# Optimization experiments

Measured on AMD Instinct MI355X. Metric: run time of the kernel, lower is better.

## Reference

```python
import jax, jax.numpy as jnp
import numpy as np

N = 32768      # total nodes
B = 64         # graphs
NPG = 512      # nodes per graph
E = 524288     # edges (avg degree 16)
H = 4          # heads
Fh = 64        # per-head dim
C = H * Fh     # 256
FIN = 128
RATIO = 0.5


def gat(x, src, dst, W, a_src, a_dst, bias, n_nodes):
    # PyG GATConv: linear -> add self-loops -> edge softmax over dst -> scatter-add
    h = (x @ W).reshape(n_nodes, H, Fh)
    loop = jnp.arange(n_nodes)
    s = jnp.concatenate([src, loop])
    d = jnp.concatenate([dst, loop])
    es = jnp.sum(h * a_src, axis=-1)  # [N,H]
    ed = jnp.sum(h * a_dst, axis=-1)  # [N,H]
    e = jax.nn.leaky_relu(es[s] + ed[d], 0.2)  # [E+N,H]
    m = jax.ops.segment_max(e, d, num_segments=n_nodes)
    ex = jnp.exp(e - m[d])
    den = jax.ops.segment_sum(ex, d, num_segments=n_nodes)
    alpha = ex / (den[d] + 1e-16)  # [E+N,H]
    out = jax.ops.segment_sum(alpha[:, :, None] * h[s], d, num_segments=n_nodes)
    return out.reshape(n_nodes, C) + bias


def pool(x, sw, sb, tw, tb, n_graphs, n_per):
    # equal-size graphs -> per-graph top-k as a batched top_k
    k = max(1, int(n_per * RATIO))
    scores = jax.nn.sigmoid(x @ sw + sb)[:, 0].reshape(n_graphs, n_per)
    _, idx = jax.lax.top_k(scores, k)  # [B,k]
    xb = x.reshape(n_graphs, n_per, x.shape[-1])
    sel = jnp.take_along_axis(xb, idx[:, :, None], axis=1)
    sel = sel.reshape(n_graphs * k, x.shape[-1])
    return sel @ tw + tb, k


def setup_inputs() -> dict:
    key = jax.random.key(0)
    ks = jax.random.split(key, 24)
    x = jax.random.normal(ks[0], (N, FIN), dtype=jnp.float32)
    # within-graph random edges
    gbase = jnp.repeat(jnp.arange(B, dtype=jnp.int32) * NPG, E // B)
    src = gbase + jax.random.randint(ks[1], (E,), 0, NPG)
    dst = gbase + jax.random.randint(ks[2], (E,), 0, NPG)
    edge_index = jnp.stack([src, dst]).astype(jnp.int32)
    batch = jnp.repeat(jnp.arange(B, dtype=jnp.int32), NPG)
    def lin(k, fi, fo):
        return jax.random.normal(k, (fi, fo), dtype=jnp.float32) / np.sqrt(fi)
    inp = dict(x=x, edge_index=edge_index, batch=batch)
    inp["W1"] = lin(ks[3], FIN, C)
    inp["a_src1"] = jax.random.normal(ks[4], (H, Fh), jnp.float32) / np.sqrt(Fh)
    inp["a_dst1"] = jax.random.normal(ks[5], (H, Fh), jnp.float32) / np.sqrt(Fh)
    inp["b1"] = jnp.zeros((C,), jnp.float32)
    inp["W2"] = lin(ks[6], C, C)
    inp["a_src2"] = jax.random.normal(ks[7], (H, Fh), jnp.float32) / np.sqrt(Fh)
    inp["a_dst2"] = jax.random.normal(ks[8], (H, Fh), jnp.float32) / np.sqrt(Fh)
    inp["b2"] = jnp.zeros((C,), jnp.float32)
    inp["p1_sw"] = lin(ks[9], C, 1)
    inp["p1_sb"] = jnp.zeros((1,), jnp.float32)
    inp["p1_tw"] = lin(ks[10], C, C)
    inp["p1_tb"] = jnp.zeros((C,), jnp.float32)
    inp["p2_sw"] = lin(ks[11], C, 1)
    inp["p2_sb"] = jnp.zeros((1,), jnp.float32)
    inp["p2_tw"] = lin(ks[12], C, C)
    inp["p2_tb"] = jnp.zeros((C,), jnp.float32)
    inp["c1w"] = lin(ks[13], C, 64)
    inp["c1b"] = jnp.zeros((64,), jnp.float32)
    inp["c2w"] = lin(ks[14], 64, 2)
    inp["c2b"] = jnp.zeros((2,), jnp.float32)
    return inp


def reference(x, edge_index, batch, W1, a_src1, a_dst1, b1, W2, a_src2, a_dst2, b2,
              p1_sw, p1_sb, p1_tw, p1_tb, p2_sw, p2_sb, p2_tw, p2_tb,
              c1w, c1b, c2w, c2b):
    src, dst = edge_index[0], edge_index[1]
    h = jax.nn.elu(gat(x, src, dst, W1, a_src1, a_dst1, b1, N))
    h = jax.nn.elu(gat(h, src, dst, W2, a_src2, a_dst2, b2, N))
    # pool1 then pool2 (edge_index after pooling is never consumed by the output path)
    h, k1 = pool(h, p1_sw, p1_sb, p1_tw, p1_tb, B, NPG)
    h, k2 = pool(h, p2_sw, p2_sb, p2_tw, p2_tb, B, k1)
    g = h.reshape(B, k2, C).mean(axis=1)  # global mean pool per graph
    g = jax.nn.relu(g @ c1w + c1b)
    g = g @ c2w + c2b
    return jax.nn.log_softmax(g, axis=1)
```

## Files before the change

### kernel.cpp

```cpp
#include <hip/hip_runtime.h>
#include <hip/hip_bf16.h>
#include <hip/hip_fp16.h>
#include <math.h>

constexpr int NN  = 32768;
constexpr int BG  = 64;
constexpr int NPG = 512;
constexpr int EG  = 524288;
constexpr int EPG = EG / BG;
constexpr int HH  = 4;
constexpr int FH  = 64;
constexpr int CC  = 256;
constexpr int FIN = 128;
constexpr int KP1 = 256;
constexpr int KP2 = 128;
constexpr int NS  = 4;

typedef __attribute__((ext_vector_type(8))) short short8;
typedef __attribute__((ext_vector_type(4))) float f32x4;

__device__ inline float leaky02(float v) { return v > 0.0f ? v : 0.2f * v; }

__device__ inline unsigned short f2bf(float v) {
    __hip_bfloat16 h = __float2bfloat16(v);
    return *(unsigned short*)&h;
}
__device__ inline float bf2f(unsigned short u) {
    __hip_bfloat16 h;
    *(unsigned short*)&h = u;
    return __bfloat162float(h);
}
__device__ inline void split2(float v, unsigned short& hi, unsigned short& lo) {
    hi = f2bf(v);
    lo = f2bf(v - bf2f(hi));
}
__device__ inline void split8(const float* p, short8& hi, short8& lo) {
    const float4 f0 = *(const float4*)p;
    const float4 f1 = *(const float4*)(p + 4);
    unsigned short h, l;
    split2(f0.x, h, l); hi[0] = (short)h; lo[0] = (short)l;
    split2(f0.y, h, l); hi[1] = (short)h; lo[1] = (short)l;
    split2(f0.z, h, l); hi[2] = (short)h; lo[2] = (short)l;
    split2(f0.w, h, l); hi[3] = (short)h; lo[3] = (short)l;
    split2(f1.x, h, l); hi[4] = (short)h; lo[4] = (short)l;
    split2(f1.y, h, l); hi[5] = (short)h; lo[5] = (short)l;
    split2(f1.z, h, l); hi[6] = (short)h; lo[6] = (short)l;
    split2(f1.w, h, l); hi[7] = (short)h; lo[7] = (short)l;
}

__device__ inline unsigned short f2h(float v) {
    __half h = __float2half(v);
    return *(unsigned short*)&h;
}

__device__ inline void acc8h(const unsigned short* p, float a, float* acc) {
    const uint4 u = *(const uint4*)p;
    const __half2* hp = (const __half2*)&u;
    const float2 f0 = __half22float2(hp[0]);
    const float2 f1 = __half22float2(hp[1]);
    const float2 f2 = __half22float2(hp[2]);
    const float2 f3 = __half22float2(hp[3]);
    acc[0] = fmaf(a, f0.x, acc[0]); acc[1] = fmaf(a, f0.y, acc[1]);
    acc[2] = fmaf(a, f1.x, acc[2]); acc[3] = fmaf(a, f1.y, acc[3]);
    acc[4] = fmaf(a, f2.x, acc[4]); acc[5] = fmaf(a, f2.y, acc[5]);
    acc[6] = fmaf(a, f3.x, acc[6]); acc[7] = fmaf(a, f3.y, acc[7]);
}

__global__ __launch_bounds__(1024) void setup_k(
        const int* __restrict__ src, const int* __restrict__ dst,
        int* __restrict__ rowp, int* __restrict__ esrc,
        const float* __restrict__ tw1, const float* __restrict__ sw2,
        const float* __restrict__ tb1, const float* __restrict__ sb2,
        float* __restrict__ w12, float* __restrict__ b12,
        const float* __restrict__ tw2, const float* __restrict__ c1w,
        const float* __restrict__ tb2, float* __restrict__ T,
        float* __restrict__ bc2,
        const float* __restrict__ W1, const float* __restrict__ W2,
        unsigned short* __restrict__ w1ph, unsigned short* __restrict__ w1pl,
        unsigned short* __restrict__ w2ph, unsigned short* __restrict__ w2pl) {
    __shared__ int lcnt[NPG];
    __shared__ int lofs[NPG];
    const int b = blockIdx.x;
    const int t = threadIdx.x;
    if (b < BG) {
        const int g = b;
        const int ebase = g * EPG;
        const int nbase = g * NPG;
        if (t < NPG) lcnt[t] = 0;
        __syncthreads();
        int ds[EPG / 1024];
#pragma unroll
        for (int j = 0; j < EPG / 1024; ++j) {
            ds[j] = dst[ebase + t + 1024 * j] - nbase;
            atomicAdd(&lcnt[ds[j]], 1);
        }
        __syncthreads();
        if (t < NPG) lofs[t] = lcnt[t];
        __syncthreads();
        for (int o = 1; o < NPG; o <<= 1) {
            int v = 0;
            if (t < NPG && t >= o) v = lofs[t - o];
            __syncthreads();
            if (t < NPG) lofs[t] += v;
            __syncthreads();
        }
        if (t < NPG) {
            int ex = lofs[t] - lcnt[t];
            rowp[nbase + t] = ebase + ex;
            lcnt[t] = ex;
        }
        if (g == BG - 1 && t == 0) rowp[NN] = EG;
        __syncthreads();
#pragma unroll
        for (int j = 0; j < EPG / 1024; ++j) {
            int p = atomicAdd(&lcnt[ds[j]], 1);
            esrc[ebase + p] = src[ebase + t + 1024 * j];
        }
        return;
    }
    if (t >= 256) return;
    const int pb = b - BG;
    if (pb < 66) {
        if (pb == 0) {
            float s = 0.0f;
            for (int o = 0; o < CC; ++o) s += tw1[t * CC + o] * sw2[o];
            w12[t] = s;
            if (t == 0) {
                float bb = 0.0f;
                for (int o = 0; o < CC; ++o) bb += tb1[o] * sw2[o];
                *b12 = bb + sb2[0];
            }
        } else if (pb < 65) {
            const int r = (pb - 1) * 4 + (t >> 6);
            const int cth = t & 63;
            float s = 0.0f;
            for (int j = 0; j < CC; ++j) s = fmaf(tw2[r * CC + j], c1w[j * 64 + cth], s);
            T[r * 64 + cth] = s;
        } else if (t < 64) {
            float s = 0.0f;
            for (int j = 0; j < CC; ++j) s = fmaf(tb2[j], c1w[j * 64 + t], s);
            bc2[t] = s;
        }
    } else {
        const int idx = (pb - 66) * 256 + t;
        if (idx < 4096) {
            const int nt = idx >> 8, rem = idx & 255;
            const int kg = rem >> 6, l = rem & 63;
            const int n = nt * 16 + (l & 15);
            const int kb = kg * 32 + (l >> 4) * 8;
            unsigned short h[8], lo[8];
#pragma unroll
            for (int j = 0; j < 8; ++j) split2(W1[(kb + j) * CC + n], h[j], lo[j]);
#pragma unroll
            for (int j = 0; j < 8; ++j) {
                w1ph[(size_t)idx * 8 + j] = h[j];
                w1pl[(size_t)idx * 8 + j] = lo[j];
            }
        } else {
            const int i2 = idx - 4096;
            const int nt = i2 >> 9, rem = i2 & 511;
            const int kg = rem >> 6, l = rem & 63;
            const int n = nt * 16 + (l & 15);
            const int kb = kg * 32 + (l >> 4) * 8;
            unsigned short h[8], lo[8];
#pragma unroll
            for (int j = 0; j < 8; ++j) split2(W2[(kb + j) * CC + n], h[j], lo[j]);
#pragma unroll
            for (int j = 0; j < 8; ++j) {
                w2ph[(size_t)i2 * 8 + j] = h[j];
                w2pl[(size_t)i2 * 8 + j] = lo[j];
            }
        }
    }
}

__global__ __launch_bounds__(256, 4) void gemm_mfma_attn(
        const unsigned short* __restrict__ Ahi, const unsigned short* __restrict__ Alo,
        const unsigned short* __restrict__ Bph, const unsigned short* __restrict__ Bpl,
        unsigned short* __restrict__ Cb, int K,
        const float* __restrict__ a_src, const float* __restrict__ a_dst,
        float* __restrict__ es, float* __restrict__ ed) {
    const int t = threadIdx.x;
    const int w = t >> 6;
    const int l = t & 63;
    const int bx   = blockIdx.x;
    const int xcd  = bx & 7;
    const int slot = bx >> 3;
    const int gph  = xcd + ((slot >> 4) << 3);
    const int row0 = gph * NPG + ((slot & 15) << 5);
    const int m = l & 15;
    const int q = l >> 4;
    const int ncol0 = w * 64;
    const int KG = K >> 5;

    const unsigned short* aH0 = Ahi + (size_t)(row0 + m) * K + q * 8;
    const unsigned short* aL0 = Alo + (size_t)(row0 + m) * K + q * 8;
    const unsigned short* aH1 = aH0 + (size_t)16 * K;
    const unsigned short* aL1 = aL0 + (size_t)16 * K;

    f32x4 acc0[4], acc1[4];
#pragma unroll
    for (int c = 0; c < 4; ++c) {
        acc0[c] = (f32x4){0.f, 0.f, 0.f, 0.f};
        acc1[c] = (f32x4){0.f, 0.f, 0.f, 0.f};
    }

    for (int kg = 0; kg < KG; ++kg) {
        const int ko = kg * 32;
        short8 ah0 = *(const short8*)(aH0 + ko);
        short8 al0 = *(const short8*)(aL0 + ko);
        short8 ah1 = *(const short8*)(aH1 + ko);
        short8 al1 = *(const short8*)(aL1 + ko);
#pragma unroll
        for (int c = 0; c < 4; ++c) {
            const int nt = (w << 2) + c;
            const size_t boff = ((size_t)(nt * KG + kg) * 64 + l) * 8;
            short8 bh = *(const short8*)(Bph + boff);
            short8 bl = *(const short8*)(Bpl + boff);
            acc0[c] = __builtin_amdgcn_mfma_f32_16x16x32_bf16(ah0, bh, acc0[c], 0, 0, 0);
            acc0[c] = __builtin_amdgcn_mfma_f32_16x16x32_bf16(ah0, bl, acc0[c], 0, 0, 0);
            acc0[c] = __builtin_amdgcn_mfma_f32_16x16x32_bf16(al0, bh, acc0[c], 0, 0, 0);
            acc1[c] = __builtin_amdgcn_mfma_f32_16x16x32_bf16(ah1, bh, acc1[c], 0, 0, 0);
            acc1[c] = __builtin_amdgcn_mfma_f32_16x16x32_bf16(ah1, bl, acc1[c], 0, 0, 0);
            acc1[c] = __builtin_amdgcn_mfma_f32_16x16x32_bf16(al1, bh, acc1[c], 0, 0, 0);
        }
    }

#pragma unroll
    for (int c = 0; c < 4; ++c)
#pragma unroll
        for (int r = 0; r < 4; ++r) {
            Cb[(size_t)(row0 + q * 4 + r) * CC + ncol0 + c * 16 + m] = f2h(acc0[c][r]);
            Cb[(size_t)(row0 + 16 + q * 4 + r) * CC + ncol0 + c * 16 + m] = f2h(acc1[c][r]);
        }

    float asv[4], adv[4];
#pragma unroll
    for (int c = 0; c < 4; ++c) {
        asv[c] = a_src[ncol0 + c * 16 + m];
        adv[c] = a_dst[ncol0 + c * 16 + m];
    }
#pragma unroll
    for (int r = 0; r < 4; ++r) {
        float ps0 = 0.f, pd0 = 0.f, ps1 = 0.f, pd1 = 0.f;
#pragma unroll
        for (int c = 0; c < 4; ++c) {
            ps0 = fmaf(acc0[c][r], asv[c], ps0);
            pd0 = fmaf(acc0[c][r], adv[c], pd0);
            ps1 = fmaf(acc1[c][r], asv[c], ps1);
            pd1 = fmaf(acc1[c][r], adv[c], pd1);
        }
#pragma unroll
        for (int o = 8; o >= 1; o >>= 1) {
            ps0 += __shfl_down(ps0, o, 16);
            pd0 += __shfl_down(pd0, o, 16);
            ps1 += __shfl_down(ps1, o, 16);
            pd1 += __shfl_down(pd1, o, 16);
        }
        if (m == 0) {
            es[(row0 + q * 4 + r) * HH + w] = ps0;
            ed[(row0 + q * 4 + r) * HH + w] = pd0;
            es[(row0 + 16 + q * 4 + r) * HH + w] = ps1;
            ed[(row0 + 16 + q * 4 + r) * HH + w] = pd1;
        }
    }
}

__global__ __launch_bounds__(256, 4) void gemm_mfma_attn_f32(
        const float* __restrict__ Af,
        const unsigned short* __restrict__ Bph, const unsigned short* __restrict__ Bpl,
        unsigned short* __restrict__ Cb, int K,
        const float* __restrict__ a_src, const float* __restrict__ a_dst,
        float* __restrict__ es, float* __restrict__ ed,
        const float* __restrict__ tw1, const float* __restrict__ T,
        const float* __restrict__ tb1, const float* __restrict__ bc2,
        const float* __restrict__ c1b, float* __restrict__ Wc,
        float* __restrict__ bcv) {
    const int t = threadIdx.x;
    const int bx = blockIdx.x;
    if (bx >= NN / 32) {
        const int fb = bx - NN / 32;
        if (fb < 64) {
            const int r = fb * 4 + (t >> 6);
            const int cth = t & 63;
            float s = 0.0f;
            for (int j = 0; j < CC; ++j) s = fmaf(tw1[r * CC + j], T[j * 64 + cth], s);
            Wc[r * 64 + cth] = s;
        } else if (t < 64) {
            float s = 0.0f;
            for (int j = 0; j < CC; ++j) s = fmaf(tb1[j], T[j * 64 + t], s);
            bcv[t] = s + bc2[t] + c1b[t];
        }
        return;
    }
    const int w = t >> 6;
    const int l = t & 63;
    const int xcd  = bx & 7;
    const int slot = bx >> 3;
    const int gph  = xcd + ((slot >> 4) << 3);
    const int row0 = gph * NPG + ((slot & 15) << 5);
    const int m = l & 15;
    const int q = l >> 4;
    const int ncol0 = w * 64;
    const int KG = K >> 5;

    const float* aF0 = Af + (size_t)(row0 + m) * K + q * 8;
    const float* aF1 = aF0 + (size_t)16 * K;

    f32x4 acc0[4], acc1[4];
#pragma unroll
    for (int c = 0; c < 4; ++c) {
        acc0[c] = (f32x4){0.f, 0.f, 0.f, 0.f};
        acc1[c] = (f32x4){0.f, 0.f, 0.f, 0.f};
    }

    for (int kg = 0; kg < KG; ++kg) {
        const int ko = kg * 32;
        short8 ah0, al0, ah1, al1;
        split8(aF0 + ko, ah0, al0);
        split8(aF1 + ko, ah1, al1);
#pragma unroll
        for (int c = 0; c < 4; ++c) {
            const int nt = (w << 2) + c;
            const size_t boff = ((size_t)(nt * KG + kg) * 64 + l) * 8;
            short8 bh = *(const short8*)(Bph + boff);
            short8 bl = *(const short8*)(Bpl + boff);
            acc0[c] = __builtin_amdgcn_mfma_f32_16x16x32_bf16(ah0, bh, acc0[c], 0, 0, 0);
            acc0[c] = __builtin_amdgcn_mfma_f32_16x16x32_bf16(ah0, bl, acc0[c], 0, 0, 0);
            acc0[c] = __builtin_amdgcn_mfma_f32_16x16x32_bf16(al0, bh, acc0[c], 0, 0, 0);
            acc1[c] = __builtin_amdgcn_mfma_f32_16x16x32_bf16(ah1, bh, acc1[c], 0, 0, 0);
            acc1[c] = __builtin_amdgcn_mfma_f32_16x16x32_bf16(ah1, bl, acc1[c], 0, 0, 0);
            acc1[c] = __builtin_amdgcn_mfma_f32_16x16x32_bf16(al1, bh, acc1[c], 0, 0, 0);
        }
    }

#pragma unroll
    for (int c = 0; c < 4; ++c)
#pragma unroll
        for (int r = 0; r < 4; ++r) {
            Cb[(size_t)(row0 + q * 4 + r) * CC + ncol0 + c * 16 + m] = f2h(acc0[c][r]);
            Cb[(size_t)(row0 + 16 + q * 4 + r) * CC + ncol0 + c * 16 + m] = f2h(acc1[c][r]);
        }

    float asv[4], adv[4];
#pragma unroll
    for (int c = 0; c < 4; ++c) {
        asv[c] = a_src[ncol0 + c * 16 + m];
        adv[c] = a_dst[ncol0 + c * 16 + m];
    }
#pragma unroll
    for (int r = 0; r < 4; ++r) {
        float ps0 = 0.f, pd0 = 0.f, ps1 = 0.f, pd1 = 0.f;
#pragma unroll
        for (int c = 0; c < 4; ++c) {
            ps0 = fmaf(acc0[c][r], asv[c], ps0);
            pd0 = fmaf(acc0[c][r], adv[c], pd0);
            ps1 = fmaf(acc1[c][r], asv[c], ps1);
            pd1 = fmaf(acc1[c][r], adv[c], pd1);
        }
#pragma unroll
        for (int o = 8; o >= 1; o >>= 1) {
            ps0 += __shfl_down(ps0, o, 16);
            pd0 += __shfl_down(pd0, o, 16);
            ps1 += __shfl_down(ps1, o, 16);
            pd1 += __shfl_down(pd1, o, 16);
        }
        if (m == 0) {
            es[(row0 + q * 4 + r) * HH + w] = ps0;
            ed[(row0 + q * 4 + r) * HH + w] = pd0;
            es[(row0 + 16 + q * 4 + r) * HH + w] = ps1;
            ed[(row0 + 16 + q * 4 + r) * HH + w] = pd1;
        }
    }
}

__global__ __launch_bounds__(256) void gat_edge(const unsigned short* __restrict__ zh,
                                                const int* __restrict__ rowp,
                                                const int* __restrict__ esrc,
                                                const float* __restrict__ es,
                                                const float* __restrict__ ed,
                                                const float* __restrict__ bias,
                                                float* __restrict__ out,
                                                unsigned short* __restrict__ outh,
                                                unsigned short* __restrict__ outl,
                                                const float* __restrict__ sw1,
                                                const float* __restrict__ sb1,
                                                const float* __restrict__ w12,
                                                const float* __restrict__ b12,
                                                float* __restrict__ sc1,
                                                float* __restrict__ sc2) {
    const int w = threadIdx.x >> 6;
    const int l = threadIdx.x & 63;
    const int b    = blockIdx.x;
    const int xcd  = b & 7;
    const int slot = b >> 3;
    const int gph  = xcd + ((slot >> 7) << 3);
    const int d    = gph * NPG + ((slot & 127) << 2) + w;

    const int h    = l & 3;
    const int ei   = l >> 2;
    const int lh   = l & 31;
    const int half = l >> 5;
    const int hcol = lh >> 3;
    const int c0   = lh << 3;

    const int beg = rowp[d];
    const int deg = rowp[d + 1] - beg;

    float acc[8];
#pragma unroll
    for (int i = 0; i < 8; ++i) acc[i] = 0.0f;

    if (deg <= 16 * NS) {
        const float edh = ed[d * HH + h];
        int   sidx[NS];
        float v[NS];
#pragma unroll
        for (int j = 0; j < NS; ++j) { sidx[j] = d; v[j] = 0.0f; }
        float vmax = -INFINITY, eself = 0.0f, vself = 0.0f;
        if (ei == 0) {
            vself = leaky02(es[d * HH + h] + edh);
            vmax = vself;
        }
#pragma unroll
        for (int j = 0; j < NS; ++j) {
            int i = ei + 16 * j;
            if (i < deg) {
                sidx[j] = esrc[beg + i];
                v[j] = leaky02(es[sidx[j] * HH + h] + edh);
                vmax = fmaxf(vmax, v[j]);
            }
        }
#pragma unroll
        for (int o = 4; o <= 32; o <<= 1) vmax = fmaxf(vmax, __shfl_xor(vmax, o));
        float dsum = 0.0f;
#pragma unroll
        for (int j = 0; j < NS; ++j) {
            int i = ei + 16 * j;
            if (i < deg) { v[j] = __expf(v[j] - vmax); dsum += v[j]; }
        }
        if (ei == 0) { eself = __expf(vself - vmax); dsum += eself; }
#pragma unroll
        for (int o = 4; o <= 32; o <<= 1) dsum += __shfl_xor(dsum, o);
        const float inv = 1.0f / (dsum + 1e-16f);
#pragma unroll
        for (int j = 0; j < NS; ++j) v[j] *= inv;
        eself *= inv;

        float aself = __shfl(eself, hcol);
        if (half) aself = 0.0f;
        acc8h(zh + (size_t)d * CC + c0, aself, acc);

#pragma unroll
        for (int j = 0; j < NS; ++j) {
            if (16 * j < deg) {
#pragma unroll
                for (int rr = 0; rr < 8; ++rr) {
                    if (16 * j + 2 * rr < deg) {
                        const int slb  = (2 * rr + half) << 2;
                        const int srcn = __shfl(sidx[j], slb);
                        const float a  = __shfl(v[j], slb + hcol);
                        acc8h(zh + (size_t)srcn * CC + c0, a, acc);
                    }
                }
            }
        }
    } else {
        const float edh = ed[d * HH + h];
        float vmax = (ei == 0) ? leaky02(es[d * HH + h] + edh) : -INFINITY;
        for (int i = ei; i < deg; i += 16)
            vmax = fmaxf(vmax, leaky02(es[esrc[beg + i] * HH + h] + edh));
#pragma unroll
        for (int o = 4; o <= 32; o <<= 1) vmax = fmaxf(vmax, __shfl_xor(vmax, o));
        float dsum = (ei == 0) ? __expf(leaky02(es[d * HH + h] + edh) - vmax) : 0.0f;
        for (int i = ei; i < deg; i += 16)
            dsum += __expf(leaky02(es[esrc[beg + i] * HH + h] + edh) - vmax);
#pragma unroll
        for (int o = 4; o <= 32; o <<= 1) dsum += __shfl_xor(dsum, o);
        const float inv = 1.0f / (dsum + 1e-16f);

        const float vmaxc = __shfl(vmax, hcol);
        const float invc  = __shfl(inv,  hcol);
        const float edh4  = ed[d * HH + hcol];
        float a0 = __expf(leaky02(es[d * HH + hcol] + edh4) - vmaxc) * invc;
        if (half) a0 = 0.0f;
        acc8h(zh + (size_t)d * CC + c0, a0, acc);
        for (int e = half; e < deg; e += 2) {
            const int srcn = esrc[beg + e];
            const float a = __expf(leaky02(es[srcn * HH + hcol] + edh4) - vmaxc) * invc;
            acc8h(zh + (size_t)srcn * CC + c0, a, acc);
        }
    }

#pragma unroll
    for (int i = 0; i < 8; ++i) acc[i] += __shfl_xor(acc[i], 32);

    const int cw = c0 + (half << 2);
    float o0 = half ? acc[4] : acc[0];
    float o1 = half ? acc[5] : acc[1];
    float o2 = half ? acc[6] : acc[2];
    float o3 = half ? acc[7] : acc[3];

    const float4 bv = *(const float4*)(bias + cw);
    o0 += bv.x; o0 = o0 > 0.0f ? o0 : expm1f(o0);
    o1 += bv.y; o1 = o1 > 0.0f ? o1 : expm1f(o1);
    o2 += bv.z; o2 = o2 > 0.0f ? o2 : expm1f(o2);
    o3 += bv.w; o3 = o3 > 0.0f ? o3 : expm1f(o3);

    if (out) *(float4*)(out + (size_t)d * CC + cw) = make_float4(o0, o1, o2, o3);
    if (outh) {
        ushort4 uh, ul;
        split2(o0, uh.x, ul.x);
        split2(o1, uh.y, ul.y);
        split2(o2, uh.z, ul.z);
        split2(o3, uh.w, ul.w);
        *(ushort4*)(outh + (size_t)d * CC + cw) = uh;
        *(ushort4*)(outl + (size_t)d * CC + cw) = ul;
    }

    if (sc1) {
        const float4 s1 = *(const float4*)(sw1 + cw);
        const float4 s2 = *(const float4*)(w12 + cw);
        float r1 = o0 * s1.x + o1 * s1.y + o2 * s1.z + o3 * s1.w;
        float r2 = o0 * s2.x + o1 * s2.y + o2 * s2.z + o3 * s2.w;
#pragma unroll
        for (int off = 32; off >= 1; off >>= 1) {
            r1 += __shfl_xor(r1, off);
            r2 += __shfl_xor(r2, off);
        }
        if (l == 0) {
            sc1[d] = r1 + sb1[0];
            sc2[d] = r2 + b12[0];
        }
    }
}

__global__ __launch_bounds__(512) void pool_head(const float* __restrict__ sc1,
                                                 const float* __restrict__ sc2,
                                                 const float* __restrict__ feat,
                                                 const float* __restrict__ Wc,
                                                 const float* __restrict__ bc,
                                                 const float* __restrict__ c2w,
                                                 const float* __restrict__ c2b,
                                                 float* __restrict__ outp) {
    __shared__ __align__(16) float s1[NPG];
    __shared__ __align__(16) float s2m[NPG];
    __shared__ int list[KP2];
    __shared__ float vbuf[2][CC];
    __shared__ float v0[CC];
    __shared__ float part[4][64];
    __shared__ float v2[64];
    const int g = blockIdx.x;
    const int t = threadIdx.x;
    s1[t] = sc1[(size_t)g * NPG + t];
    const float mys2 = sc2[(size_t)g * NPG + t];
    __syncthreads();
    {
        const float my = s1[t];
        int rank = 0;
#pragma unroll 16
        for (int j4 = 0; j4 < NPG / 4; ++j4) {
            const float4 sv = *(const float4*)(s1 + j4 * 4);
            const int jb = j4 * 4;
            rank += (sv.x > my) || (sv.x == my && (jb + 0) < t);
            rank += (sv.y > my) || (sv.y == my && (jb + 1) < t);
            rank += (sv.z > my) || (sv.z == my && (jb + 2) < t);
            rank += (sv.w > my) || (sv.w == my && (jb + 3) < t);
        }
        s2m[t] = (rank < KP1) ? mys2 : -INFINITY;
    }
    __syncthreads();
    {
        const float my = s2m[t];
        int rank = 0;
#pragma unroll 16
        for (int j4 = 0; j4 < NPG / 4; ++j4) {
            const float4 sv = *(const float4*)(s2m + j4 * 4);
            const int jb = j4 * 4;
            rank += (sv.x > my) || (sv.x == my && (jb + 0) < t);
            rank += (sv.y > my) || (sv.y == my && (jb + 1) < t);
            rank += (sv.z > my) || (sv.z == my && (jb + 2) < t);
            rank += (sv.w > my) || (sv.w == my && (jb + 3) < t);
        }
        if (rank < KP2 && my != -INFINITY) list[rank] = t;
    }
    __syncthreads();
    {
        const int col = t & (CC - 1);
        const int nh  = t >> 8;
        float acc = 0.0f;
#pragma unroll 4
        for (int i = nh * 64; i < nh * 64 + 64; ++i) {
            const int n = list[i];
            acc += feat[((size_t)g * NPG + n) * CC + col];
        }
        vbuf[nh][col] = acc;
    }
    __syncthreads();
    if (t < CC) v0[t] = (vbuf[0][t] + vbuf[1][t]) * (1.0f / KP2);
    __syncthreads();
    if (t < 256) {
        const int q = t >> 6, cth = t & 63;
        float p = 0.0f;
        for (int j = q * 64; j < q * 64 + 64; ++j)
            p = fmaf(v0[j], Wc[j * 64 + cth], p);
        part[q][cth] = p;
    }
    __syncthreads();
    if (t < 64) {
        float u = bc[t];
#pragma unroll
        for (int q = 0; q < 4; ++q) u += part[q][t];
        v2[t] = fmaxf(u, 0.0f);
    }
    __syncthreads();
    if (t < 2) {
        float o = c2b[t];
        for (int j = 0; j < 64; ++j) o = fmaf(v2[j], c2w[j * 2 + t], o);
        part[0][t] = o;
    }
    __syncthreads();
    if (t == 0) {
        float a = part[0][0], bq = part[0][1];
        float mx = fmaxf(a, bq);
        float lse = mx + logf(expf(a - mx) + expf(bq - mx));
        outp[g * 2 + 0] = a - lse;
        outp[g * 2 + 1] = bq - lse;
    }
}

extern "C" void kernel_launch(void* const* d_in, const int* in_sizes, int n_in,
                              void* d_out, int out_size, void* d_ws, size_t ws_size,
                              hipStream_t stream) {
    const float* x      = (const float*)d_in[0];
    const int*   ei     = (const int*)d_in[1];
    const int*   src    = ei;
    const int*   dst    = ei + EG;
    const float* W1     = (const float*)d_in[3];
    const float* a_src1 = (const float*)d_in[4];
    const float* a_dst1 = (const float*)d_in[5];
    const float* b1     = (const float*)d_in[6];
    const float* W2     = (const float*)d_in[7];
    const float* a_src2 = (const float*)d_in[8];
    const float* a_dst2 = (const float*)d_in[9];
    const float* b2     = (const float*)d_in[10];
    const float* p1_sw  = (const float*)d_in[11];
    const float* p1_sb  = (const float*)d_in[12];
    const float* p1_tw  = (const float*)d_in[13];
    const float* p1_tb  = (const float*)d_in[14];
    const float* p2_sw  = (const float*)d_in[15];
    const float* p2_sb  = (const float*)d_in[16];
    const float* p2_tw  = (const float*)d_in[17];
    const float* p2_tb  = (const float*)d_in[18];
    const float* c1w    = (const float*)d_in[19];
    const float* c1b    = (const float*)d_in[20];
    const float* c2w    = (const float*)d_in[21];
    const float* c2b    = (const float*)d_in[22];
    float* out = (float*)d_out;

    float* ws = (float*)d_ws;
    float* z = ws;
    unsigned short* zh = (unsigned short*)z;
    float* fregion = z + (size_t)NN * CC;
    unsigned short* fhi = (unsigned short*)fregion;
    unsigned short* flo = fhi + (size_t)NN * CC;
    float* featF = fregion;
    float* wsp = fregion + (size_t)NN * CC;
    unsigned short* w1ph = (unsigned short*)wsp;
    unsigned short* w1pl = w1ph + 256 * FIN;
    unsigned short* w2ph = w1pl + 256 * FIN;
    unsigned short* w2pl = w2ph + 256 * CC;
    float* es  = (float*)(w2pl + 256 * CC);
    float* ed  = es + NN * HH;
    int* rowp  = (int*)(ed + NN * HH);
    int* esrc  = rowp + NN + 1;
    float* sc1 = (float*)(esrc + EG);
    float* sc2 = sc1 + NN;
    int* sel1  = (int*)(sc2 + NN);
    float* w12 = (float*)(sel1 + NN);
    float* b12 = w12 + CC;
    float* T   = b12 + 64;
    float* Wc  = T + CC * 64;
    float* bc2 = Wc + CC * 64;
    float* bcv = bc2 + 64;

    setup_k<<<BG + 66 + 48, 1024, 0, stream>>>(
        src, dst, rowp, esrc,
        p1_tw, p2_sw, p1_tb, p2_sb, w12, b12, p2_tw, c1w, p2_tb, T, bc2,
        W1, W2, w1ph, w1pl, w2ph, w2pl);

    gemm_mfma_attn_f32<<<NN / 32 + 65, 256, 0, stream>>>(
        x, w1ph, w1pl, zh, FIN, a_src1, a_dst1, es, ed,
        p1_tw, T, p1_tb, bc2, c1b, Wc, bcv);
    gat_edge<<<NN / 4, 256, 0, stream>>>(zh, rowp, esrc, es, ed, b1,
                                         nullptr, fhi, flo,
                                         nullptr, nullptr, nullptr, nullptr,
                                         nullptr, nullptr);

    gemm_mfma_attn<<<NN / 32, 256, 0, stream>>>(fhi, flo, w2ph, w2pl, zh, CC,
                                                a_src2, a_dst2, es, ed);
    gat_edge<<<NN / 4, 256, 0, stream>>>(zh, rowp, esrc, es, ed, b2,
                                         featF, nullptr, nullptr,
                                         p1_sw, p1_sb, w12, b12, sc1, sc2);

    pool_head<<<BG, 512, 0, stream>>>(sc1, sc2, featF, Wc, bcv, c2w, c2b, out);
}
```

Before: 277.2 us.

## Split pooling head across four blocks per graph with last-block reduction

The final pool/head kernel now runs four 256-thread blocks per graph instead of one 512-thread block. Each block recomputes the first-stage top-k ranks, then ranks its own quarter of nodes for the second stage, masks kept nodes, and sums their features into a partial vector. An atomic counter (zeroed in setup) picks the last block per graph to combine partials and run the classifier head. This spreads a 64-block tail kernel over more CUs, at the cost of redundant rank work, extra global traffic for partials, and fence/atomic synchronisation.

```diff
diff --git a/kernel.cpp b/kernel.cpp
--- a/kernel.cpp
+++ b/kernel.cpp
@@ -77,7 +77,8 @@
         float* __restrict__ bc2,
         const float* __restrict__ W1, const float* __restrict__ W2,
         unsigned short* __restrict__ w1ph, unsigned short* __restrict__ w1pl,
-        unsigned short* __restrict__ w2ph, unsigned short* __restrict__ w2pl) {
+        unsigned short* __restrict__ w2ph, unsigned short* __restrict__ w2pl,
+        int* __restrict__ cnt) {
     __shared__ int lcnt[NPG];
     __shared__ int lofs[NPG];
     const int b = blockIdx.x;
@@ -122,6 +123,7 @@
     const int pb = b - BG;
     if (pb < 66) {
         if (pb == 0) {
+            if (t < BG) cnt[t] = 0;
             float s = 0.0f;
             for (int o = 0; o < CC; ++o) s += tw1[t * CC + o] * sw2[o];
             w12[t] = s;
@@ -535,76 +537,111 @@
     }
 }
 
-__global__ __launch_bounds__(512) void pool_head(const float* __restrict__ sc1,
-                                                 const float* __restrict__ sc2,
-                                                 const float* __restrict__ feat,
-                                                 const float* __restrict__ Wc,
-                                                 const float* __restrict__ bc,
-                                                 const float* __restrict__ c2w,
-                                                 const float* __restrict__ c2b,
-                                                 float* __restrict__ outp) {
+__global__ __launch_bounds__(256) void pool_k(const float* __restrict__ sc1,
+                                              const float* __restrict__ sc2,
+                                              const float* __restrict__ feat,
+                                              const float* __restrict__ Wc,
+                                              const float* __restrict__ bc,
+                                              const float* __restrict__ c2w,
+                                              const float* __restrict__ c2b,
+                                              float* __restrict__ partial,
+                                              int* __restrict__ cnt,
+                                              float* __restrict__ outp) {
     __shared__ __align__(16) float s1[NPG];
-    __shared__ __align__(16) float s2m[NPG];
-    __shared__ int list[KP2];
-    __shared__ float vbuf[2][CC];
-    __shared__ float v0[CC];
+    __shared__ __align__(16) float s2[NPG];
+    __shared__ int rk2[2][128];
+    __shared__ int keep[128];
+    __shared__ float vbuf[4][CC];
     __shared__ float part[4][64];
     __shared__ float v2[64];
-    const int g = blockIdx.x;
+    __shared__ int lastf;
+    const int b = blockIdx.x;
+    const int g = b >> 2, p = b & 3;
     const int t = threadIdx.x;
-    s1[t] = sc1[(size_t)g * NPG + t];
-    const float mys2 = sc2[(size_t)g * NPG + t];
+    s1[t]       = sc1[(size_t)g * NPG + t];
+    s1[t + 256] = sc1[(size_t)g * NPG + t + 256];
+    s2[t]       = sc2[(size_t)g * NPG + t];
+    s2[t + 256] = sc2[(size_t)g * NPG + t + 256];
     __syncthreads();
     {
-        const float my = s1[t];
-        int rank = 0;
-#pragma unroll 16
+        const float my0 = s1[t];
+        const float my1 = s1[t + 256];
+        const int n1 = t + 256;
+        int r0 = 0, r1 = 0;
+#pragma unroll 8
         for (int j4 = 0; j4 < NPG / 4; ++j4) {
             const float4 sv = *(const float4*)(s1 + j4 * 4);
             const int jb = j4 * 4;
-            rank += (sv.x > my) || (sv.x == my && (jb + 0) < t);
-            rank += (sv.y > my) || (sv.y == my && (jb + 1) < t);
-            rank += (sv.z > my) || (sv.z == my && (jb + 2) < t);
-            rank += (sv.w > my) || (sv.w == my && (jb + 3) < t);
-        }
-        s2m[t] = (rank < KP1) ? mys2 : -INFINITY;
+            r0 += (sv.x > my0) || (sv.x == my0 && (jb + 0) < t);
+            r0 += (sv.y > my0) || (sv.y == my0 && (jb + 1) < t);
+            r0 += (sv.z > my0) || (sv.z == my0 && (jb + 2) < t);
+            r0 += (sv.w > my0) || (sv.w == my0 && (jb + 3) < t);
+            r1 += (sv.x > my1) || (sv.x == my1 && (jb + 0) < n1);
+            r1 += (sv.y > my1) || (sv.y == my1 && (jb + 1) < n1);
+            r1 += (sv.z > my1) || (sv.z == my1 && (jb + 2) < n1);
+            r1 += (sv.w > my1) || (sv.w == my1 && (jb + 3) < n1);
+        }
+        if (r0 >= KP1) s2[t] = -INFINITY;
+        if (r1 >= KP1) s2[n1] = -INFINITY;
     }
     __syncthreads();
     {
-        const float my = s2m[t];
-        int rank = 0;
-#pragma unroll 16
-        for (int j4 = 0; j4 < NPG / 4; ++j4) {
-            const float4 sv = *(const float4*)(s2m + j4 * 4);
-            const int jb = j4 * 4;
-            rank += (sv.x > my) || (sv.x == my && (jb + 0) < t);
-            rank += (sv.y > my) || (sv.y == my && (jb + 1) < t);
-            rank += (sv.z > my) || (sv.z == my && (jb + 2) < t);
-            rank += (sv.w > my) || (sv.w == my && (jb + 3) < t);
-        }
-        if (rank < KP2 && my != -INFINITY) list[rank] = t;
-    }
+        const int n = p * 128 + (t & 127);
+        const int hf = t >> 7;
+        const float my = s2[n];
+        const int base = hf * 256;
+        int rr = 0;
+#pragma unroll 8
+        for (int j4 = 0; j4 < 64; ++j4) {
+            const float4 sv = *(const float4*)(s2 + base + j4 * 4);
+            const int jb = base + j4 * 4;
+            rr += (sv.x > my) || (sv.x == my && (jb + 0) < n);
+            rr += (sv.y > my) || (sv.y == my && (jb + 1) < n);
+            rr += (sv.z > my) || (sv.z == my && (jb + 2) < n);
+            rr += (sv.w > my) || (sv.w == my && (jb + 3) < n);
+        }
+        rk2[hf][t & 127] = rr;
+    }
+    __syncthreads();
+    if (t < 128)
+        keep[t] = (rk2[0][t] + rk2[1][t] < KP2) && (s2[p * 128 + t] != -INFINITY);
     __syncthreads();
     {
-        const int col = t & (CC - 1);
-        const int nh  = t >> 8;
-        float acc = 0.0f;
-#pragma unroll 4
-        for (int i = nh * 64; i < nh * 64 + 64; ++i) {
-            const int n = list[i];
-            acc += feat[((size_t)g * NPG + n) * CC + col];
-        }
-        vbuf[nh][col] = acc;
-    }
-    __syncthreads();
-    if (t < CC) v0[t] = (vbuf[0][t] + vbuf[1][t]) * (1.0f / KP2);
-    __syncthreads();
-    if (t < 256) {
+        const int r = t >> 6, c4 = t & 63;
+        float4 acc = make_float4(0.f, 0.f, 0.f, 0.f);
+        const float4* f4 = (const float4*)(feat + ((size_t)g * NPG + p * 128) * CC);
+        for (int j = r; j < 128; j += 4) {
+            if (keep[j]) {
+                float4 v = f4[j * 64 + c4];
+                acc.x += v.x; acc.y += v.y; acc.z += v.z; acc.w += v.w;
+            }
+        }
+        vbuf[r][c4 * 4 + 0] = acc.x;
+        vbuf[r][c4 * 4 + 1] = acc.y;
+        vbuf[r][c4 * 4 + 2] = acc.z;
+        vbuf[r][c4 * 4 + 3] = acc.w;
+    }
+    __syncthreads();
+    partial[(size_t)(g * 4 + p) * CC + t] =
+        vbuf[0][t] + vbuf[1][t] + vbuf[2][t] + vbuf[3][t];
+    __threadfence();
+    __syncthreads();
+    if (t == 0) lastf = (atomicAdd(&cnt[g], 1) == 3);
+    __syncthreads();
+    if (!lastf) return;
+    __threadfence();
+    float tsum = partial[(size_t)(g * 4 + 0) * CC + t] +
+                 partial[(size_t)(g * 4 + 1) * CC + t] +
+                 partial[(size_t)(g * 4 + 2) * CC + t] +
+                 partial[(size_t)(g * 4 + 3) * CC + t];
+    s1[t] = tsum * (1.0f / KP2);
+    __syncthreads();
+    {
         const int q = t >> 6, cth = t & 63;
-        float p = 0.0f;
+        float pr = 0.0f;
         for (int j = q * 64; j < q * 64 + 64; ++j)
-            p = fmaf(v0[j], Wc[j * 64 + cth], p);
-        part[q][cth] = p;
+            pr = fmaf(s1[j], Wc[j * 64 + cth], pr);
+        part[q][cth] = pr;
     }
     __syncthreads();
     if (t < 64) {
@@ -683,11 +720,13 @@
     float* Wc  = T + CC * 64;
     float* bc2 = Wc + CC * 64;
     float* bcv = bc2 + 64;
+    float* partial = bcv + 64;
+    int*   cnt = (int*)(partial + (size_t)BG * 4 * CC);
 
     setup_k<<<BG + 66 + 48, 1024, 0, stream>>>(
         src, dst, rowp, esrc,
         p1_tw, p2_sw, p1_tb, p2_sb, w12, b12, p2_tw, c1w, p2_tb, T, bc2,
-        W1, W2, w1ph, w1pl, w2ph, w2pl);
+        W1, W2, w1ph, w1pl, w2ph, w2pl, cnt);
 
     gemm_mfma_attn_f32<<<NN / 32 + 65, 256, 0, stream>>>(
         x, w1ph, w1pl, zh, FIN, a_src1, a_dst1, es, ed,
@@ -703,5 +742,6 @@
                                          featF, nullptr, nullptr,
                                          p1_sw, p1_sb, w12, b12, sc1, sc2);
 
-    pool_head<<<BG, 512, 0, stream>>>(sc1, sc2, featF, Wc, bcv, c2w, c2b, out);
-}
+    pool_k<<<BG * 4, 256, 0, stream>>>(sc1, sc2, featF, Wc, bcv, c2w, c2b,
+                                       partial, cnt, out);
+}
```

Measured after the change: 302.6 us. 1.09x slower.

## Replace O(n^2) rank-count top-k with radix bit-select using wave ballots

Applied to the files above, without the earlier changes.

The pooling kernel's two top-k selections change from each thread counting how many of 512 scores beat it to a 32-step radix select on order-preserving uint keys. Each step counts candidates with wave ballots and a per-wave shared-memory reduction. Ties are broken by index through a prefix count, and the kept list is built by ballot compaction, so node order becomes index order rather than rank order. This cuts per-thread compare work but adds about 70 block barriers, which may cost more than the compare loops for a small 64-block kernel.

```diff
diff --git a/kernel.cpp b/kernel.cpp
--- a/kernel.cpp
+++ b/kernel.cpp
@@ -51,6 +51,11 @@
 __device__ inline unsigned short f2h(float v) {
     __half h = __float2half(v);
     return *(unsigned short*)&h;
+}
+
+__device__ inline unsigned int fmap(float v) {
+    unsigned int b = __float_as_uint(v);
+    return (b & 0x80000000u) ? ~b : (b | 0x80000000u);
 }
 
 __device__ inline void acc8h(const unsigned short* p, float a, float* acc) {
@@ -535,76 +540,128 @@
     }
 }
 
-__global__ __launch_bounds__(512) void pool_head(const float* __restrict__ sc1,
-                                                 const float* __restrict__ sc2,
-                                                 const float* __restrict__ feat,
-                                                 const float* __restrict__ Wc,
-                                                 const float* __restrict__ bc,
-                                                 const float* __restrict__ c2w,
-                                                 const float* __restrict__ c2b,
-                                                 float* __restrict__ outp) {
-    __shared__ __align__(16) float s1[NPG];
-    __shared__ __align__(16) float s2m[NPG];
+__global__ __launch_bounds__(512) void pool_g(const float* __restrict__ sc1,
+                                              const float* __restrict__ sc2,
+                                              const float* __restrict__ feat,
+                                              const float* __restrict__ Wc,
+                                              const float* __restrict__ bc,
+                                              const float* __restrict__ c2w,
+                                              const float* __restrict__ c2b,
+                                              float* __restrict__ outp) {
+    __shared__ int wcnt[2][8];
+    __shared__ int ecnt[8];
+    __shared__ int ccnt[8];
     __shared__ int list[KP2];
+    __shared__ float v0[CC];
     __shared__ float vbuf[2][CC];
-    __shared__ float v0[CC];
     __shared__ float part[4][64];
     __shared__ float v2[64];
     const int g = blockIdx.x;
     const int t = threadIdx.x;
-    s1[t] = sc1[(size_t)g * NPG + t];
-    const float mys2 = sc2[(size_t)g * NPG + t];
+    const int lane = t & 63, wid = t >> 6;
+    const unsigned long long lmask = (1ull << lane) - 1ull;
+
+    const unsigned int u1 = fmap(sc1[(size_t)g * NPG + t]);
+    unsigned int p = 0;
+    int pp = 0;
+    for (int bb = 31; bb >= 0; --bb) {
+        const unsigned int cand = p | (1u << bb);
+        unsigned long long bal = __ballot(u1 >= cand);
+        if (lane == 0) wcnt[pp][wid] = __popcll(bal);
+        __syncthreads();
+        int c = 0;
+#pragma unroll
+        for (int i = 0; i < 8; ++i) c += wcnt[pp][i];
+        if (c >= KP1) p = cand;
+        pp ^= 1;
+    }
+    int cgt;
+    {
+        unsigned long long bal = __ballot(u1 > p);
+        if (lane == 0) wcnt[pp][wid] = __popcll(bal);
+        __syncthreads();
+        cgt = 0;
+#pragma unroll
+        for (int i = 0; i < 8; ++i) cgt += wcnt[pp][i];
+        pp ^= 1;
+    }
+    int keep1;
+    {
+        const int eq = (u1 == p);
+        unsigned long long bal = __ballot(eq);
+        if (lane == 0) ecnt[wid] = __popcll(bal);
+        __syncthreads();
+        int pre = 0;
+        for (int i = 0; i < wid; ++i) pre += ecnt[i];
+        const int eqrank = pre + __popcll(bal & lmask);
+        keep1 = (u1 > p) || (eq && eqrank < (KP1 - cgt));
+    }
     __syncthreads();
+
+    const unsigned int u2 = keep1 ? fmap(sc2[(size_t)g * NPG + t]) : 0u;
+    p = 0;
+    for (int bb = 31; bb >= 0; --bb) {
+        const unsigned int cand = p | (1u << bb);
+        unsigned long long bal = __ballot(u2 >= cand);
+        if (lane == 0) wcnt[pp][wid] = __popcll(bal);
+        __syncthreads();
+        int c = 0;
+#pragma unroll
+        for (int i = 0; i < 8; ++i) c += wcnt[pp][i];
+        if (c >= KP2) p = cand;
+        pp ^= 1;
+    }
     {
-        const float my = s1[t];
-        int rank = 0;
-#pragma unroll 16
-        for (int j4 = 0; j4 < NPG / 4; ++j4) {
-            const float4 sv = *(const float4*)(s1 + j4 * 4);
-            const int jb = j4 * 4;
-            rank += (sv.x > my) || (sv.x == my && (jb + 0) < t);
-            rank += (sv.y > my) || (sv.y == my && (jb + 1) < t);
-            rank += (sv.z > my) || (sv.z == my && (jb + 2) < t);
-            rank += (sv.w > my) || (sv.w == my && (jb + 3) < t);
-        }
-        s2m[t] = (rank < KP1) ? mys2 : -INFINITY;
+        unsigned long long bal = __ballot(u2 > p);
+        if (lane == 0) wcnt[pp][wid] = __popcll(bal);
+        __syncthreads();
+        cgt = 0;
+#pragma unroll
+        for (int i = 0; i < 8; ++i) cgt += wcnt[pp][i];
+        pp ^= 1;
+    }
+    int keep2;
+    {
+        const int eq = (u2 == p);
+        unsigned long long bal = __ballot(eq);
+        if (lane == 0) ccnt[wid] = __popcll(bal);
+        __syncthreads();
+        int pre = 0;
+        for (int i = 0; i < wid; ++i) pre += ccnt[i];
+        const int eqrank = pre + __popcll(bal & lmask);
+        keep2 = (u2 > p) || (eq && eqrank < (KP2 - cgt));
     }
     __syncthreads();
+
     {
-        const float my = s2m[t];
-        int rank = 0;
-#pragma unroll 16
-        for (int j4 = 0; j4 < NPG / 4; ++j4) {
-            const float4 sv = *(const float4*)(s2m + j4 * 4);
-            const int jb = j4 * 4;
-            rank += (sv.x > my) || (sv.x == my && (jb + 0) < t);
-            rank += (sv.y > my) || (sv.y == my && (jb + 1) < t);
-            rank += (sv.z > my) || (sv.z == my && (jb + 2) < t);
-            rank += (sv.w > my) || (sv.w == my && (jb + 3) < t);
-        }
-        if (rank < KP2 && my != -INFINITY) list[rank] = t;
+        unsigned long long bal = __ballot(keep2);
+        if (lane == 0) ecnt[wid] = __popcll(bal);
+        __syncthreads();
+        int pre = 0;
+        for (int i = 0; i < wid; ++i) pre += ecnt[i];
+        const int pos = pre + __popcll(bal & lmask);
+        if (keep2) list[pos] = t;
     }
     __syncthreads();
+
     {
         const int col = t & (CC - 1);
-        const int nh  = t >> 8;
+        const int hf = t >> 8;
         float acc = 0.0f;
-#pragma unroll 4
-        for (int i = nh * 64; i < nh * 64 + 64; ++i) {
-            const int n = list[i];
-            acc += feat[((size_t)g * NPG + n) * CC + col];
-        }
-        vbuf[nh][col] = acc;
+        for (int i = hf * 64; i < hf * 64 + 64; ++i)
+            acc += feat[((size_t)g * NPG + list[i]) * CC + col];
+        vbuf[hf][col] = acc;
     }
     __syncthreads();
     if (t < CC) v0[t] = (vbuf[0][t] + vbuf[1][t]) * (1.0f / KP2);
     __syncthreads();
+
     if (t < 256) {
         const int q = t >> 6, cth = t & 63;
-        float p = 0.0f;
+        float pr = 0.0f;
         for (int j = q * 64; j < q * 64 + 64; ++j)
-            p = fmaf(v0[j], Wc[j * 64 + cth], p);
-        part[q][cth] = p;
+            pr = fmaf(v0[j], Wc[j * 64 + cth], pr);
+        part[q][cth] = pr;
     }
     __syncthreads();
     if (t < 64) {
@@ -703,5 +760,5 @@
                                          featF, nullptr, nullptr,
                                          p1_sw, p1_sb, w12, b12, sc1, sc2);
 
-    pool_head<<<BG, 512, 0, stream>>>(sc1, sc2, featF, Wc, bcv, c2w, c2b, out);
-}
+    pool_g<<<BG, 512, 0, stream>>>(sc1, sc2, featF, Wc, bcv, c2w, c2b, out);
+}
```

Measured after the change: 265.7 us. 4.1% less time.
